# Optimization experiments

Hardware: AMD Instinct MI355X
Metric: run time of the kernel (lower is better)

The kernel has to match this reference:

```python
import jax, jax.numpy as jnp
import numpy as np

IN_FEAT, HIDDEN, OUT_FEAT = 2048, 1024, 2048
CODEBOOK_DIM, NUM_CODES = 32, 256
B, S = 4, 4096


def setup_inputs() -> dict:
    key = jax.random.key(0)
    ks = jax.random.split(key, 10)
    sc = lambda fan_in: 1.0 / np.sqrt(fan_in)
    return {
        "x": jax.random.normal(ks[0], (B, S, IN_FEAT), dtype=jnp.float32),
        # down: Linear(in_feat, hidden)
        "down_w": jax.random.normal(ks[1], (HIDDEN, IN_FEAT), dtype=jnp.float32) * sc(IN_FEAT),
        "down_b": jax.random.normal(ks[2], (HIDDEN,), dtype=jnp.float32) * sc(IN_FEAT),
        # VQ project_in: Linear(hidden, codebook_dim)
        "pin_w": jax.random.normal(ks[3], (CODEBOOK_DIM, HIDDEN), dtype=jnp.float32) * sc(HIDDEN),
        "pin_b": jax.random.normal(ks[4], (CODEBOOK_DIM,), dtype=jnp.float32) * sc(HIDDEN),
        # codebook embeddings
        "codebook": jax.random.normal(ks[5], (NUM_CODES, CODEBOOK_DIM), dtype=jnp.float32),
        # VQ project_out: Linear(codebook_dim, hidden)
        "pout_w": jax.random.normal(ks[6], (HIDDEN, CODEBOOK_DIM), dtype=jnp.float32) * sc(CODEBOOK_DIM),
        "pout_b": jax.random.normal(ks[7], (HIDDEN,), dtype=jnp.float32) * sc(CODEBOOK_DIM),
        # up: Linear(hidden, out_feat)
        "up_w": jax.random.normal(ks[8], (OUT_FEAT, HIDDEN), dtype=jnp.float32) * sc(HIDDEN),
        "up_b": jax.random.normal(ks[9], (OUT_FEAT,), dtype=jnp.float32) * sc(HIDDEN),
    }


def reference(x, down_w, down_b, pin_w, pin_b, codebook, pout_w, pout_b, up_w, up_b):
    # down-proj: [B,S,in] -> [B,S,hidden]
    h = jnp.einsum("bsi,hi->bsh", x, down_w) + down_b
    # VQ project_in: [B,S,hidden] -> [B,S,codebook_dim]
    z = jnp.einsum("bsh,ch->bsc", h, pin_w) + pin_b
    # squared euclidean distances to codebook: [B,S,num_codes]
    dist = (
        jnp.sum(z * z, axis=-1, keepdims=True)
        - 2.0 * jnp.einsum("bsc,nc->bsn", z, codebook)
        + jnp.sum(codebook * codebook, axis=-1)
    )
    indices = jnp.argmin(dist, axis=-1)  # [B,S] int
    quant = codebook[indices]            # [B,S,codebook_dim]
    # straight-through estimator
    quant = z + jax.lax.stop_gradient(quant - z)
    # VQ project_out: -> [B,S,hidden]
    hq = jnp.einsum("bsc,hc->bsh", quant, pout_w) + pout_b
    # up-proj: -> [B,S,out]
    out = jnp.einsum("bsh,oh->bso", hq, up_w) + up_b
    commit_loss = jnp.zeros((), dtype=x.dtype)  # commitment_weight = 0
    return jnp.clip(out, -1.0, 1.0), indices, commit_loss
```

## Files before the change

kernel.cpp:

```cpp
#include <hip/hip_runtime.h>

#define TOK   16384
#define INFT  2048
#define HID   1024
#define CBD   32
#define NC    256
#define OUTF  2048
#define KB    4

#define WS_UPWT   0
#define WS_ZPART  0
#define WS_PART1  2097152
#define WS_T      2097152
#define WS_WFT    3145728
#define WS_BF     3211264
#define WS_BPART  3211296
#define WS_PART2  3311648

__global__ __launch_bounds__(256) void k_stage1(
    const float* __restrict__ up_w, const float* __restrict__ pin_w,
    const float* __restrict__ pin_b, const float* __restrict__ down_w,
    const float* __restrict__ down_b, float* __restrict__ ws) {
    int bid = blockIdx.x, tid = threadIdx.x;
    if (bid < 2048) {
        __shared__ float tile[32][33];
        float* up_wT = ws + WS_UPWT;
        int h0 = (bid & 31) * 32;
        int o0 = (bid >> 5) * 32;
        int tx = tid & 31, ty = tid >> 5;
        #pragma unroll
        for (int j = 0; j < 32; j += 8)
            tile[ty + j][tx] = up_w[(o0 + ty + j) * HID + h0 + tx];
        __syncthreads();
        #pragma unroll
        for (int j = 0; j < 32; j += 8)
            up_wT[(h0 + ty + j) * OUTF + o0 + tx] = tile[tx][ty + j];
    } else if (bid < 2176) {
        float* part1 = ws + WS_PART1;
        int b  = bid - 2048;
        int i  = (b & 7) * 256 + tid;
        int k0 = (b >> 3) * 64;
        float acc[32];
        #pragma unroll
        for (int c = 0; c < 32; c++) acc[c] = 0.f;
        #pragma unroll 4
        for (int j = 0; j < 64; j++) {
            float xv = down_w[(k0 + j) * 2048 + i];
            #pragma unroll
            for (int c = 0; c < 32; c++)
                acc[c] = fmaf(pin_w[c * HID + k0 + j], xv, acc[c]);
        }
        #pragma unroll
        for (int c = 0; c < 32; c++)
            part1[((b >> 3) * 32 + c) * 2048 + i] = acc[c];
    } else {
        __shared__ float red[256];
        float* bf = ws + WS_BF;
        int c = tid >> 3, seg = tid & 7;
        float s = 0.f;
        #pragma unroll 8
        for (int k = seg * 128; k < seg * 128 + 128; k++)
            s = fmaf(pin_w[c * HID + k], down_b[k], s);
        red[tid] = s;
        __syncthreads();
        if (tid < 32) {
            float t = pin_b[tid];
            #pragma unroll
            for (int q = 0; q < 8; q++) t += red[tid * 8 + q];
            bf[tid] = t;
        }
    }
}

__global__ __launch_bounds__(256) void k_stage2(
    const float* __restrict__ pout_w, const float* __restrict__ pout_b,
    const float* __restrict__ up_b, float* __restrict__ ws) {
    int bid = blockIdx.x, tid = threadIdx.x;
    if (bid < 256) {
        const float* part1 = ws + WS_PART1;
        float* WfT = ws + WS_WFT;
        int f = bid * 256 + tid;
        int i = f & 2047, c = f >> 11;
        float s = 0.f;
        #pragma unroll
        for (int b = 0; b < 16; b++) s += part1[b * 65536 + c * 2048 + i];
        WfT[i * 32 + c] = s;
    } else {
        const float* up_wT = ws + WS_UPWT;
        float* part2 = ws + WS_PART2;
        float* bpart = ws + WS_BPART;
        int b  = bid - 256;
        int i  = (b & 7) * 256 + tid;
        int hc = b >> 3;
        int k0 = hc * 128;
        float acc[32];
        #pragma unroll
        for (int c = 0; c < 32; c++) acc[c] = 0.f;
        float accb = 0.f;
        #pragma unroll 4
        for (int j = 0; j < 128; j++) {
            float xv = up_wT[(k0 + j) * 2048 + i];
            accb = fmaf(pout_b[k0 + j], xv, accb);
            #pragma unroll
            for (int c = 0; c < 32; c++)
                acc[c] = fmaf(pout_w[(k0 + j) * 32 + c], xv, acc[c]);
        }
        #pragma unroll
        for (int c = 0; c < 32; c++)
            part2[(hc * 32 + c) * 2048 + i] = acc[c];
        bpart[hc * 2048 + i] = accb + (hc == 0 ? up_b[i] : 0.f);
    }
}

__global__ __launch_bounds__(256) void k_stage3(
    const float* __restrict__ x, const float* __restrict__ cb,
    float* __restrict__ ws) {
    __shared__ float4 xs[64 * 33 + 1];
    int bid = blockIdx.x, tid = threadIdx.x;
    if (bid < 64) {
        const float* part2 = ws + WS_PART2;
        const float* bpart = ws + WS_BPART;
        float* T = ws + WS_T;
        int o  = (bid & 7) * 256 + tid;
        int n0 = (bid >> 3) * 32;
        float u[32];
        #pragma unroll
        for (int c = 0; c < 32; c++) {
            float s = 0.f;
            #pragma unroll
            for (int kc = 0; kc < 8; kc++)
                s += part2[(kc * 32 + c) * 2048 + o];
            u[c] = s;
        }
        float bsum = 0.f;
        #pragma unroll
        for (int hc = 0; hc < 8; hc++) bsum += bpart[hc * 2048 + o];
        for (int n = n0; n < n0 + 32; n++) {
            float s = bsum;
            #pragma unroll
            for (int c = 0; c < 32; c++)
                s = fmaf(cb[n * 32 + c], u[c], s);
            T[n * 2048 + o] = s;
        }
    } else {
        const float* WfT = ws + WS_WFT;
        float* zpart = ws + WS_ZPART;
        int b    = bid - 64;
        int lane = tid & 63;
        int w    = __builtin_amdgcn_readfirstlane(tid >> 6);
        int m0   = (b & 255) * 64;
        int kb   = b >> 8;

        float acc[32];
        #pragma unroll
        for (int c = 0; c < 32; c++) acc[c] = 0.f;

        for (int sc = 0; sc < 4; sc++) {
            int k0 = kb * 512 + sc * 128;
            #pragma unroll
            for (int j = 0; j < 8; j++) {
                int f = j * 256 + tid;
                int t = f >> 5, q = f & 31;
                xs[t * 33 + q] = *(const float4*)(x + (size_t)(m0 + t) * 2048 + k0 + q * 4);
            }
            __syncthreads();
            const float* wr = WfT + (size_t)(k0 + w * 32) * 32;
            #pragma unroll 2
            for (int j = 0; j < 8; j++) {
                float4 xv = xs[lane * 33 + w * 8 + j];
                #pragma unroll
                for (int c = 0; c < 32; c++) {
                    acc[c] = fmaf(wr[(j * 4 + 0) * 32 + c], xv.x, acc[c]);
                    acc[c] = fmaf(wr[(j * 4 + 1) * 32 + c], xv.y, acc[c]);
                    acc[c] = fmaf(wr[(j * 4 + 2) * 32 + c], xv.z, acc[c]);
                    acc[c] = fmaf(wr[(j * 4 + 3) * 32 + c], xv.w, acc[c]);
                }
            }
            __syncthreads();
        }

        float* rp = (float*)xs;
        #pragma unroll
        for (int c = 0; c < 32; c++)
            rp[(w * 64 + lane) * 33 + c] = acc[c];
        __syncthreads();
        int t  = tid >> 2;
        int cq = (tid & 3) * 8;
        float s[8];
        #pragma unroll
        for (int j = 0; j < 8; j++) {
            float v = rp[(0 * 64 + t) * 33 + cq + j];
            #pragma unroll
            for (int ww = 1; ww < 4; ww++) v += rp[(ww * 64 + t) * 33 + cq + j];
            s[j] = v;
        }
        float* zp = zpart + ((size_t)kb * TOK + m0 + t) * 32 + cq;
        *(float4*)zp       = make_float4(s[0], s[1], s[2], s[3]);
        *(float4*)(zp + 4) = make_float4(s[4], s[5], s[6], s[7]);
    }
}

__global__ __launch_bounds__(256) void k_stage4(
    const float* __restrict__ cb, const float* __restrict__ ws,
    float* __restrict__ out, float* __restrict__ idx_f, float* __restrict__ loss) {
    __shared__ float z_s[64 * 36];
    __shared__ float cbs[256 * 36];
    __shared__ float cbn[256];
    __shared__ float red_d[256];
    __shared__ int   red_i[256];
    __shared__ int   idx_s[64];

    const float* zpart = ws + WS_ZPART;
    const float* bf    = ws + WS_BF;
    const float* T     = ws + WS_T;

    int tid  = threadIdx.x;
    int lane = tid & 63;
    int w    = __builtin_amdgcn_readfirstlane(tid >> 6);
    int m0   = blockIdx.x * 64;

    #pragma unroll
    for (int i = 0; i < 8; i++) {
        int f = i * 256 + tid;
        int t = f >> 5, c = f & 31;
        float s = bf[c];
        #pragma unroll
        for (int kb = 0; kb < KB; kb++)
            s += zpart[((size_t)kb * TOK + m0 + t) * 32 + c];
        z_s[t * 36 + c] = s;
    }
    #pragma unroll
    for (int j = 0; j < 8; j++) {
        int f = j * 256 + tid;
        int n = f >> 3, q = f & 7;
        float4 v = *(const float4*)(cb + n * 32 + q * 4);
        cbs[n * 36 + q * 4 + 0] = v.x;
        cbs[n * 36 + q * 4 + 1] = v.y;
        cbs[n * 36 + q * 4 + 2] = v.z;
        cbs[n * 36 + q * 4 + 3] = v.w;
    }
    __syncthreads();
    {
        float s = 0.f;
        #pragma unroll
        for (int q = 0; q < 8; q++) {
            float4 v = *(const float4*)(&cbs[tid * 36 + q * 4]);
            s += v.x * v.x + v.y * v.y + v.z * v.z + v.w * v.w;
        }
        cbn[tid] = s;
    }
    __syncthreads();

    float z[32];
    #pragma unroll
    for (int q = 0; q < 8; q++) {
        float4 v = *(const float4*)(&z_s[lane * 36 + q * 4]);
        z[q * 4 + 0] = v.x; z[q * 4 + 1] = v.y; z[q * 4 + 2] = v.z; z[q * 4 + 3] = v.w;
    }
    float bd = 3.4e38f; int bi = 0;
    for (int t = 0; t < 64; t++) {
        int n = w * 64 + t;
        float s = 0.f;
        #pragma unroll
        for (int q = 0; q < 8; q++) {
            float4 v = *(const float4*)(&cbs[n * 36 + q * 4]);
            s = fmaf(v.x, z[q * 4 + 0], s);
            s = fmaf(v.y, z[q * 4 + 1], s);
            s = fmaf(v.z, z[q * 4 + 2], s);
            s = fmaf(v.w, z[q * 4 + 3], s);
        }
        float d = fmaf(-2.f, s, cbn[n]);
        if (d < bd) { bd = d; bi = n; }
    }
    red_d[w * 64 + lane] = bd;
    red_i[w * 64 + lane] = bi;
    __syncthreads();
    if (tid < 64) {
        float d0 = red_d[tid]; int i0 = red_i[tid];
        #pragma unroll
        for (int ww = 1; ww < 4; ww++) {
            float d1 = red_d[ww * 64 + tid];
            int   i1 = red_i[ww * 64 + tid];
            if (d1 < d0) { d0 = d1; i0 = i1; }
        }
        idx_s[tid] = i0;
        idx_f[m0 + tid] = (float)i0;
    }
    __syncthreads();

    const float4* T4 = (const float4*)T;
    float4* O4 = (float4*)(out + (size_t)m0 * 2048);
    #pragma unroll 2
    for (int r = 0; r < 64; r++) {
        int n = idx_s[r];
        const float4* Tr = T4 + (size_t)n * 512;
        float4 v0 = Tr[tid];
        float4 v1 = Tr[256 + tid];
        v0.x = fminf(fmaxf(v0.x, -1.f), 1.f);
        v0.y = fminf(fmaxf(v0.y, -1.f), 1.f);
        v0.z = fminf(fmaxf(v0.z, -1.f), 1.f);
        v0.w = fminf(fmaxf(v0.w, -1.f), 1.f);
        v1.x = fminf(fmaxf(v1.x, -1.f), 1.f);
        v1.y = fminf(fmaxf(v1.y, -1.f), 1.f);
        v1.z = fminf(fmaxf(v1.z, -1.f), 1.f);
        v1.w = fminf(fmaxf(v1.w, -1.f), 1.f);
        O4[(size_t)r * 512 + tid]       = v0;
        O4[(size_t)r * 512 + 256 + tid] = v1;
    }
    if (blockIdx.x == 0 && tid == 0) *loss = 0.f;
}

extern "C" void kernel_launch(void* const* d_in, const int* in_sizes, int n_in,
                              void* d_out, int out_size, void* d_ws, size_t ws_size,
                              hipStream_t stream) {
    const float* x      = (const float*)d_in[0];
    const float* down_w = (const float*)d_in[1];
    const float* down_b = (const float*)d_in[2];
    const float* pin_w  = (const float*)d_in[3];
    const float* pin_b  = (const float*)d_in[4];
    const float* cb     = (const float*)d_in[5];
    const float* pout_w = (const float*)d_in[6];
    const float* pout_b = (const float*)d_in[7];
    const float* up_w   = (const float*)d_in[8];
    const float* up_b   = (const float*)d_in[9];

    float* ws = (float*)d_ws;
    float* out_f  = (float*)d_out;
    float* idx_f  = out_f + (size_t)TOK * OUTF;
    float* loss_f = idx_f + TOK;

    k_stage1<<<2177, 256, 0, stream>>>(up_w, pin_w, pin_b, down_w, down_b, ws);
    k_stage2<<<320,  256, 0, stream>>>(pout_w, pout_b, up_b, ws);
    k_stage3<<<1088, 256, 0, stream>>>(x, cb, ws);
    k_stage4<<<256,  256, 0, stream>>>(cb, ws, out_f, idx_f, loss_f);
}
```

Before: 391.3 us.

## Fuse z-projection GEMM with argmin/gather kernel and register-prefetch x tiles

Splits the former stage3 into a small table-building kernel and merges the fused x·Wf projection into the argmin/gather kernel, so each block computes its full 2048-long reduction itself instead of writing split-K partials to workspace. The x tile for the next chunk is prefetched into registers while the current chunk is computed. This removes the zpart round-trip and one split-K reduction, but cuts the projection grid from 1024 blocks to 256, which means less parallelism and latency hiding on a GPU with many compute units.

```diff
diff --git a/kernel.cpp b/kernel.cpp
--- a/kernel.cpp
+++ b/kernel.cpp
@@ -6,10 +6,8 @@
 #define CBD   32
 #define NC    256
 #define OUTF  2048
-#define KB    4
 
 #define WS_UPWT   0
-#define WS_ZPART  0
 #define WS_PART1  2097152
 #define WS_T      2097152
 #define WS_WFT    3145728
@@ -112,59 +110,103 @@
     }
 }
 
-__global__ __launch_bounds__(256) void k_stage3(
+__global__ __launch_bounds__(256) void k_table(
+    const float* __restrict__ cb, float* __restrict__ ws) {
+    const float* part2 = ws + WS_PART2;
+    const float* bpart = ws + WS_BPART;
+    float* T = ws + WS_T;
+    int bid = blockIdx.x, tid = threadIdx.x;
+    int o  = (bid & 7) * 256 + tid;
+    int n0 = (bid >> 3) * 32;
+    float u[32];
+    #pragma unroll
+    for (int c = 0; c < 32; c++) {
+        float s = 0.f;
+        #pragma unroll
+        for (int kc = 0; kc < 8; kc++)
+            s += part2[(kc * 32 + c) * 2048 + o];
+        u[c] = s;
+    }
+    float bsum = 0.f;
+    #pragma unroll
+    for (int hc = 0; hc < 8; hc++) bsum += bpart[hc * 2048 + o];
+    for (int n = n0; n < n0 + 32; n++) {
+        float s = bsum;
+        #pragma unroll
+        for (int c = 0; c < 32; c++)
+            s = fmaf(cb[n * 32 + c], u[c], s);
+        T[n * 2048 + o] = s;
+    }
+}
+
+__global__ __launch_bounds__(256) void k_main(
     const float* __restrict__ x, const float* __restrict__ cb,
-    float* __restrict__ ws) {
-    __shared__ float4 xs[64 * 33 + 1];
-    int bid = blockIdx.x, tid = threadIdx.x;
-    if (bid < 64) {
-        const float* part2 = ws + WS_PART2;
-        const float* bpart = ws + WS_BPART;
-        float* T = ws + WS_T;
-        int o  = (bid & 7) * 256 + tid;
-        int n0 = (bid >> 3) * 32;
-        float u[32];
-        #pragma unroll
-        for (int c = 0; c < 32; c++) {
-            float s = 0.f;
-            #pragma unroll
-            for (int kc = 0; kc < 8; kc++)
-                s += part2[(kc * 32 + c) * 2048 + o];
-            u[c] = s;
-        }
-        float bsum = 0.f;
-        #pragma unroll
-        for (int hc = 0; hc < 8; hc++) bsum += bpart[hc * 2048 + o];
-        for (int n = n0; n < n0 + 32; n++) {
-            float s = bsum;
-            #pragma unroll
-            for (int c = 0; c < 32; c++)
-                s = fmaf(cb[n * 32 + c], u[c], s);
-            T[n * 2048 + o] = s;
-        }
-    } else {
-        const float* WfT = ws + WS_WFT;
-        float* zpart = ws + WS_ZPART;
-        int b    = bid - 64;
-        int lane = tid & 63;
-        int w    = __builtin_amdgcn_readfirstlane(tid >> 6);
-        int m0   = (b & 255) * 64;
-        int kb   = b >> 8;
-
-        float acc[32];
-        #pragma unroll
-        for (int c = 0; c < 32; c++) acc[c] = 0.f;
-
+    const float* __restrict__ ws, float* __restrict__ out,
+    float* __restrict__ idx_f, float* __restrict__ loss) {
+    __shared__ __align__(16) char pool[49408];
+    float4* xs   = (float4*)pool;
+    float*  cbs  = (float*)pool;
+    float*  z_s  = (float*)(pool + 36864);
+    float*  cbn  = (float*)(pool + 46080);
+    float*  red_d = (float*)(pool + 47104);
+    int*    red_i = (int*)(pool + 48128);
+    int*    idx_s = (int*)(pool + 49152);
+
+    const float* WfT = ws + WS_WFT;
+    const float* bf  = ws + WS_BF;
+    const float* T   = ws + WS_T;
+
+    int tid  = threadIdx.x;
+    int lane = tid & 63;
+    int w    = __builtin_amdgcn_readfirstlane(tid >> 6);
+    int m0   = blockIdx.x * 64;
+    const float* xb = x + (size_t)m0 * 2048;
+
+    int tt = tid >> 2;
+    int cq = (tid & 3) * 8;
+
+    float bfv[8];
+    {
+        float4 b0 = *(const float4*)(bf + cq);
+        float4 b1 = *(const float4*)(bf + cq + 4);
+        bfv[0] = b0.x; bfv[1] = b0.y; bfv[2] = b0.z; bfv[3] = b0.w;
+        bfv[4] = b1.x; bfv[5] = b1.y; bfv[6] = b1.z; bfv[7] = b1.w;
+    }
+
+    float acc[32];
+    #pragma unroll
+    for (int c = 0; c < 32; c++) acc[c] = 0.f;
+    float stotal[8];
+
+    float4 r[8];
+    #pragma unroll
+    for (int j = 0; j < 8; j++) {
+        int f = j * 256 + tid;
+        int t = f >> 5, q = f & 31;
+        r[j] = *(const float4*)(xb + (size_t)t * 2048 + q * 4);
+    }
+
+    for (int kb = 0; kb < 4; kb++) {
         for (int sc = 0; sc < 4; sc++) {
-            int k0 = kb * 512 + sc * 128;
+            int ch = kb * 4 + sc;
+            __syncthreads();
             #pragma unroll
             for (int j = 0; j < 8; j++) {
                 int f = j * 256 + tid;
                 int t = f >> 5, q = f & 31;
-                xs[t * 33 + q] = *(const float4*)(x + (size_t)(m0 + t) * 2048 + k0 + q * 4);
+                xs[t * 33 + q] = r[j];
             }
             __syncthreads();
-            const float* wr = WfT + (size_t)(k0 + w * 32) * 32;
+            if (ch < 15) {
+                int k0n = (ch + 1) * 128;
+                #pragma unroll
+                for (int j = 0; j < 8; j++) {
+                    int f = j * 256 + tid;
+                    int t = f >> 5, q = f & 31;
+                    r[j] = *(const float4*)(xb + (size_t)t * 2048 + k0n + q * 4);
+                }
+            }
+            const float* wr = WfT + (size_t)(ch * 128 + w * 32) * 32;
             #pragma unroll 2
             for (int j = 0; j < 8; j++) {
                 float4 xv = xs[lane * 33 + w * 8 + j];
@@ -176,59 +218,29 @@
                     acc[c] = fmaf(wr[(j * 4 + 3) * 32 + c], xv.w, acc[c]);
                 }
             }
-            __syncthreads();
-        }
-
+        }
+        __syncthreads();
         float* rp = (float*)xs;
         #pragma unroll
         for (int c = 0; c < 32; c++)
             rp[(w * 64 + lane) * 33 + c] = acc[c];
         __syncthreads();
-        int t  = tid >> 2;
-        int cq = (tid & 3) * 8;
-        float s[8];
         #pragma unroll
         for (int j = 0; j < 8; j++) {
-            float v = rp[(0 * 64 + t) * 33 + cq + j];
-            #pragma unroll
-            for (int ww = 1; ww < 4; ww++) v += rp[(ww * 64 + t) * 33 + cq + j];
-            s[j] = v;
-        }
-        float* zp = zpart + ((size_t)kb * TOK + m0 + t) * 32 + cq;
-        *(float4*)zp       = make_float4(s[0], s[1], s[2], s[3]);
-        *(float4*)(zp + 4) = make_float4(s[4], s[5], s[6], s[7]);
-    }
-}
-
-__global__ __launch_bounds__(256) void k_stage4(
-    const float* __restrict__ cb, const float* __restrict__ ws,
-    float* __restrict__ out, float* __restrict__ idx_f, float* __restrict__ loss) {
-    __shared__ float z_s[64 * 36];
-    __shared__ float cbs[256 * 36];
-    __shared__ float cbn[256];
-    __shared__ float red_d[256];
-    __shared__ int   red_i[256];
-    __shared__ int   idx_s[64];
-
-    const float* zpart = ws + WS_ZPART;
-    const float* bf    = ws + WS_BF;
-    const float* T     = ws + WS_T;
-
-    int tid  = threadIdx.x;
-    int lane = tid & 63;
-    int w    = __builtin_amdgcn_readfirstlane(tid >> 6);
-    int m0   = blockIdx.x * 64;
-
-    #pragma unroll
-    for (int i = 0; i < 8; i++) {
-        int f = i * 256 + tid;
-        int t = f >> 5, c = f & 31;
-        float s = bf[c];
-        #pragma unroll
-        for (int kb = 0; kb < KB; kb++)
-            s += zpart[((size_t)kb * TOK + m0 + t) * 32 + c];
-        z_s[t * 36 + c] = s;
-    }
+            float v = rp[(0 * 64 + tt) * 33 + cq + j];
+            #pragma unroll
+            for (int ww = 1; ww < 4; ww++) v += rp[(ww * 64 + tt) * 33 + cq + j];
+            float base = (kb == 0) ? bfv[j] : stotal[j];
+            stotal[j] = base + v;
+        }
+        #pragma unroll
+        for (int c = 0; c < 32; c++) acc[c] = 0.f;
+    }
+
+    *(float4*)(z_s + tt * 36 + cq)     = make_float4(stotal[0], stotal[1], stotal[2], stotal[3]);
+    *(float4*)(z_s + tt * 36 + cq + 4) = make_float4(stotal[4], stotal[5], stotal[6], stotal[7]);
+    __syncthreads();
+
     #pragma unroll
     for (int j = 0; j < 8; j++) {
         int f = j * 256 + tid;
@@ -291,8 +303,8 @@
     const float4* T4 = (const float4*)T;
     float4* O4 = (float4*)(out + (size_t)m0 * 2048);
     #pragma unroll 2
-    for (int r = 0; r < 64; r++) {
-        int n = idx_s[r];
+    for (int rr = 0; rr < 64; rr++) {
+        int n = idx_s[rr];
         const float4* Tr = T4 + (size_t)n * 512;
         float4 v0 = Tr[tid];
         float4 v1 = Tr[256 + tid];
@@ -304,8 +316,8 @@
         v1.y = fminf(fmaxf(v1.y, -1.f), 1.f);
         v1.z = fminf(fmaxf(v1.z, -1.f), 1.f);
         v1.w = fminf(fmaxf(v1.w, -1.f), 1.f);
-        O4[(size_t)r * 512 + tid]       = v0;
-        O4[(size_t)r * 512 + 256 + tid] = v1;
+        O4[(size_t)rr * 512 + tid]       = v0;
+        O4[(size_t)rr * 512 + 256 + tid] = v1;
     }
     if (blockIdx.x == 0 && tid == 0) *loss = 0.f;
 }
@@ -331,6 +343,6 @@
 
     k_stage1<<<2177, 256, 0, stream>>>(up_w, pin_w, pin_b, down_w, down_b, ws);
     k_stage2<<<320,  256, 0, stream>>>(pout_w, pout_b, up_b, ws);
-    k_stage3<<<1088, 256, 0, stream>>>(x, cb, ws);
-    k_stage4<<<256,  256, 0, stream>>>(cb, ws, out_f, idx_f, loss_f);
-}
+    k_table<<<64,   256, 0, stream>>>(cb, ws);
+    k_main<<<256,   256, 0, stream>>>(x, cb, ws, out_f, idx_f, loss_f);
+}
```

New measurement: 543.9 us. +39.0%, slower.

## Split table and z-GEMM kernels, prefetch x tiles into registers

Applied to the files above, without the earlier changes.

The fused stage3 kernel, which branched on block id between building the output table and running the x·Wf GEMM, becomes two separate kernels. The GEMM kernel now loads the next 128-wide slice of x into registers while computing on the current slice in shared memory, a register double-buffering scheme. It also sets launch_bounds occupancy hint 4 and uses a 2D grid. This aims to hide global load latency and remove branch divergence between roles. The cost is higher register pressure and an extra kernel launch, and the small table kernel no longer overlaps with the GEMM.

```diff
diff --git a/kernel.cpp b/kernel.cpp
--- a/kernel.cpp
+++ b/kernel.cpp
@@ -112,96 +112,114 @@
     }
 }
 
-__global__ __launch_bounds__(256) void k_stage3(
-    const float* __restrict__ x, const float* __restrict__ cb,
-    float* __restrict__ ws) {
+__global__ __launch_bounds__(256) void k_table(
+    const float* __restrict__ cb, float* __restrict__ ws) {
+    const float* part2 = ws + WS_PART2;
+    const float* bpart = ws + WS_BPART;
+    float* T = ws + WS_T;
+    int bid = blockIdx.x, tid = threadIdx.x;
+    int o  = (bid & 7) * 256 + tid;
+    int n0 = (bid >> 3) * 32;
+    float u[32];
+    #pragma unroll
+    for (int c = 0; c < 32; c++) {
+        float s = 0.f;
+        #pragma unroll
+        for (int kc = 0; kc < 8; kc++)
+            s += part2[(kc * 32 + c) * 2048 + o];
+        u[c] = s;
+    }
+    float bsum = 0.f;
+    #pragma unroll
+    for (int hc = 0; hc < 8; hc++) bsum += bpart[hc * 2048 + o];
+    for (int n = n0; n < n0 + 32; n++) {
+        float s = bsum;
+        #pragma unroll
+        for (int c = 0; c < 32; c++)
+            s = fmaf(cb[n * 32 + c], u[c], s);
+        T[n * 2048 + o] = s;
+    }
+}
+
+__global__ __launch_bounds__(256, 4) void k_zgemm(
+    const float* __restrict__ x, const float* __restrict__ WfT,
+    float* __restrict__ zpart) {
     __shared__ float4 xs[64 * 33 + 1];
-    int bid = blockIdx.x, tid = threadIdx.x;
-    if (bid < 64) {
-        const float* part2 = ws + WS_PART2;
-        const float* bpart = ws + WS_BPART;
-        float* T = ws + WS_T;
-        int o  = (bid & 7) * 256 + tid;
-        int n0 = (bid >> 3) * 32;
-        float u[32];
-        #pragma unroll
-        for (int c = 0; c < 32; c++) {
-            float s = 0.f;
-            #pragma unroll
-            for (int kc = 0; kc < 8; kc++)
-                s += part2[(kc * 32 + c) * 2048 + o];
-            u[c] = s;
-        }
-        float bsum = 0.f;
-        #pragma unroll
-        for (int hc = 0; hc < 8; hc++) bsum += bpart[hc * 2048 + o];
-        for (int n = n0; n < n0 + 32; n++) {
-            float s = bsum;
-            #pragma unroll
-            for (int c = 0; c < 32; c++)
-                s = fmaf(cb[n * 32 + c], u[c], s);
-            T[n * 2048 + o] = s;
-        }
-    } else {
-        const float* WfT = ws + WS_WFT;
-        float* zpart = ws + WS_ZPART;
-        int b    = bid - 64;
-        int lane = tid & 63;
-        int w    = __builtin_amdgcn_readfirstlane(tid >> 6);
-        int m0   = (b & 255) * 64;
-        int kb   = b >> 8;
-
-        float acc[32];
-        #pragma unroll
-        for (int c = 0; c < 32; c++) acc[c] = 0.f;
-
-        for (int sc = 0; sc < 4; sc++) {
-            int k0 = kb * 512 + sc * 128;
+    int tid  = threadIdx.x;
+    int lane = tid & 63;
+    int w    = __builtin_amdgcn_readfirstlane(tid >> 6);
+    int m0   = blockIdx.x * 64;
+    int kb   = blockIdx.y;
+    const float* xb = x + (size_t)m0 * 2048 + kb * 512;
+
+    float acc[32];
+    #pragma unroll
+    for (int c = 0; c < 32; c++) acc[c] = 0.f;
+
+    float4 r[8];
+    #pragma unroll
+    for (int j = 0; j < 8; j++) {
+        int f = j * 256 + tid;
+        int t = f >> 5, q = f & 31;
+        r[j] = *(const float4*)(xb + (size_t)t * 2048 + q * 4);
+    }
+
+    for (int sc = 0; sc < 4; sc++) {
+        __syncthreads();
+        #pragma unroll
+        for (int j = 0; j < 8; j++) {
+            int f = j * 256 + tid;
+            int t = f >> 5, q = f & 31;
+            xs[t * 33 + q] = r[j];
+        }
+        __syncthreads();
+        if (sc < 3) {
+            int k0n = (sc + 1) * 128;
             #pragma unroll
             for (int j = 0; j < 8; j++) {
                 int f = j * 256 + tid;
                 int t = f >> 5, q = f & 31;
-                xs[t * 33 + q] = *(const float4*)(x + (size_t)(m0 + t) * 2048 + k0 + q * 4);
+                r[j] = *(const float4*)(xb + (size_t)t * 2048 + k0n + q * 4);
             }
-            __syncthreads();
-            const float* wr = WfT + (size_t)(k0 + w * 32) * 32;
-            #pragma unroll 2
-            for (int j = 0; j < 8; j++) {
-                float4 xv = xs[lane * 33 + w * 8 + j];
-                #pragma unroll
-                for (int c = 0; c < 32; c++) {
-                    acc[c] = fmaf(wr[(j * 4 + 0) * 32 + c], xv.x, acc[c]);
-                    acc[c] = fmaf(wr[(j * 4 + 1) * 32 + c], xv.y, acc[c]);
-                    acc[c] = fmaf(wr[(j * 4 + 2) * 32 + c], xv.z, acc[c]);
-                    acc[c] = fmaf(wr[(j * 4 + 3) * 32 + c], xv.w, acc[c]);
-                }
+        }
+        const float* wr = WfT + (size_t)(kb * 512 + sc * 128 + w * 32) * 32;
+        #pragma unroll 2
+        for (int j = 0; j < 8; j++) {
+            float4 xv = xs[lane * 33 + w * 8 + j];
+            #pragma unroll
+            for (int c = 0; c < 32; c++) {
+                acc[c] = fmaf(wr[(j * 4 + 0) * 32 + c], xv.x, acc[c]);
+                acc[c] = fmaf(wr[(j * 4 + 1) * 32 + c], xv.y, acc[c]);
+                acc[c] = fmaf(wr[(j * 4 + 2) * 32 + c], xv.z, acc[c]);
+                acc[c] = fmaf(wr[(j * 4 + 3) * 32 + c], xv.w, acc[c]);
             }
-            __syncthreads();
-        }
-
-        float* rp = (float*)xs;
-        #pragma unroll
-        for (int c = 0; c < 32; c++)
-            rp[(w * 64 + lane) * 33 + c] = acc[c];
-        __syncthreads();
-        int t  = tid >> 2;
-        int cq = (tid & 3) * 8;
-        float s[8];
-        #pragma unroll
-        for (int j = 0; j < 8; j++) {
-            float v = rp[(0 * 64 + t) * 33 + cq + j];
-            #pragma unroll
-            for (int ww = 1; ww < 4; ww++) v += rp[(ww * 64 + t) * 33 + cq + j];
-            s[j] = v;
-        }
-        float* zp = zpart + ((size_t)kb * TOK + m0 + t) * 32 + cq;
-        *(float4*)zp       = make_float4(s[0], s[1], s[2], s[3]);
-        *(float4*)(zp + 4) = make_float4(s[4], s[5], s[6], s[7]);
-    }
+        }
+    }
+
+    __syncthreads();
+    float* rp = (float*)xs;
+    #pragma unroll
+    for (int c = 0; c < 32; c++)
+        rp[(w * 64 + lane) * 33 + c] = acc[c];
+    __syncthreads();
+    int t  = tid >> 2;
+    int cq = (tid & 3) * 8;
+    float s[8];
+    #pragma unroll
+    for (int j = 0; j < 8; j++) {
+        float v = rp[(0 * 64 + t) * 33 + cq + j];
+        #pragma unroll
+        for (int ww = 1; ww < 4; ww++) v += rp[(ww * 64 + t) * 33 + cq + j];
+        s[j] = v;
+    }
+    float* zp = zpart + ((size_t)kb * TOK + m0 + t) * 32 + cq;
+    *(float4*)zp       = make_float4(s[0], s[1], s[2], s[3]);
+    *(float4*)(zp + 4) = make_float4(s[4], s[5], s[6], s[7]);
 }
 
 __global__ __launch_bounds__(256) void k_stage4(
-    const float* __restrict__ cb, const float* __restrict__ ws,
+    const float* __restrict__ zpart, const float* __restrict__ bf,
+    const float* __restrict__ T, const float* __restrict__ cb,
     float* __restrict__ out, float* __restrict__ idx_f, float* __restrict__ loss) {
     __shared__ float z_s[64 * 36];
     __shared__ float cbs[256 * 36];
@@ -209,10 +227,6 @@
     __shared__ float red_d[256];
     __shared__ int   red_i[256];
     __shared__ int   idx_s[64];
-
-    const float* zpart = ws + WS_ZPART;
-    const float* bf    = ws + WS_BF;
-    const float* T     = ws + WS_T;
 
     int tid  = threadIdx.x;
     int lane = tid & 63;
@@ -291,8 +305,8 @@
     const float4* T4 = (const float4*)T;
     float4* O4 = (float4*)(out + (size_t)m0 * 2048);
     #pragma unroll 2
-    for (int r = 0; r < 64; r++) {
-        int n = idx_s[r];
+    for (int rr = 0; rr < 64; rr++) {
+        int n = idx_s[rr];
         const float4* Tr = T4 + (size_t)n * 512;
         float4 v0 = Tr[tid];
         float4 v1 = Tr[256 + tid];
@@ -304,8 +318,8 @@
         v1.y = fminf(fmaxf(v1.y, -1.f), 1.f);
         v1.z = fminf(fmaxf(v1.z, -1.f), 1.f);
         v1.w = fminf(fmaxf(v1.w, -1.f), 1.f);
-        O4[(size_t)r * 512 + tid]       = v0;
-        O4[(size_t)r * 512 + 256 + tid] = v1;
+        O4[(size_t)rr * 512 + tid]       = v0;
+        O4[(size_t)rr * 512 + 256 + tid] = v1;
     }
     if (blockIdx.x == 0 && tid == 0) *loss = 0.f;
 }
@@ -325,12 +339,18 @@
     const float* up_b   = (const float*)d_in[9];
 
     float* ws = (float*)d_ws;
+    float* zpart = ws + WS_ZPART;
+    float* WfT   = ws + WS_WFT;
+    float* bf    = ws + WS_BF;
+    float* T     = ws + WS_T;
+
     float* out_f  = (float*)d_out;
     float* idx_f  = out_f + (size_t)TOK * OUTF;
     float* loss_f = idx_f + TOK;
 
     k_stage1<<<2177, 256, 0, stream>>>(up_w, pin_w, pin_b, down_w, down_b, ws);
     k_stage2<<<320,  256, 0, stream>>>(pout_w, pout_b, up_b, ws);
-    k_stage3<<<1088, 256, 0, stream>>>(x, cb, ws);
-    k_stage4<<<256,  256, 0, stream>>>(cb, ws, out_f, idx_f, loss_f);
-}
+    k_table<<<64,    256, 0, stream>>>(cb, ws);
+    k_zgemm<<<dim3(256, KB), 256, 0, stream>>>(x, WfT, zpart);
+    k_stage4<<<256,  256, 0, stream>>>(zpart, bf, T, cb, out_f, idx_f, loss_f);
+}
```

New measurement: 451.2 us. 15.3% more time.

## Double-buffer x tiles via direct global-to-LDS loads with XOR swizzle

Applied to the files above, without the earlier changes.

The x-projection GEMV in the third stage now stages x chunks straight into LDS with global_load_lds and double-buffers them, so the load of the next 128-column chunk overlaps compute on the current one. A padded layout is replaced by an XOR swizzle to avoid bank conflicts, and launch bounds request 4 blocks per CU. The costs are twice the shared memory for the x tiles and some register pressure from the occupancy hint. Stage 4 now takes explicit pointers instead of workspace offsets.

```diff
diff --git a/kernel.cpp b/kernel.cpp
--- a/kernel.cpp
+++ b/kernel.cpp
@@ -112,10 +112,25 @@
     }
 }
 
-__global__ __launch_bounds__(256) void k_stage3(
+#define STAGE_CHUNK(dstbuf, ch_)                                              \
+    {                                                                         \
+        const float* sb_ = xb + (ch_) * 128;                                  \
+        _Pragma("unroll")                                                     \
+        for (int j = 0; j < 8; j++) {                                         \
+            int row_  = (w * 8 + j) * 2 + (lane >> 5);                        \
+            int clog_ = (lane & 31) ^ (row_ & 31);                            \
+            const float* srcp_ = sb_ + (size_t)row_ * 2048 + clog_ * 4;       \
+            __builtin_amdgcn_global_load_lds(                                 \
+                (const __attribute__((address_space(1))) void*)srcp_,         \
+                (__attribute__((address_space(3))) void*)((dstbuf) + (w * 8 + j) * 64), \
+                16, 0, 0);                                                    \
+        }                                                                     \
+    }
+
+__global__ __launch_bounds__(256, 4) void k_zmain(
     const float* __restrict__ x, const float* __restrict__ cb,
-    float* __restrict__ ws) {
-    __shared__ float4 xs[64 * 33 + 1];
+    const float* __restrict__ WfT, float* __restrict__ ws) {
+    __shared__ float4 buf2[2][64 * 32];
     int bid = blockIdx.x, tid = threadIdx.x;
     if (bid < 64) {
         const float* part2 = ws + WS_PART2;
@@ -142,66 +157,66 @@
                 s = fmaf(cb[n * 32 + c], u[c], s);
             T[n * 2048 + o] = s;
         }
-    } else {
-        const float* WfT = ws + WS_WFT;
-        float* zpart = ws + WS_ZPART;
-        int b    = bid - 64;
-        int lane = tid & 63;
-        int w    = __builtin_amdgcn_readfirstlane(tid >> 6);
-        int m0   = (b & 255) * 64;
-        int kb   = b >> 8;
-
-        float acc[32];
-        #pragma unroll
-        for (int c = 0; c < 32; c++) acc[c] = 0.f;
-
-        for (int sc = 0; sc < 4; sc++) {
-            int k0 = kb * 512 + sc * 128;
-            #pragma unroll
-            for (int j = 0; j < 8; j++) {
-                int f = j * 256 + tid;
-                int t = f >> 5, q = f & 31;
-                xs[t * 33 + q] = *(const float4*)(x + (size_t)(m0 + t) * 2048 + k0 + q * 4);
+        return;
+    }
+
+    float* zpart = ws + WS_ZPART;
+    int b    = bid - 64;
+    int lane = tid & 63;
+    int w    = __builtin_amdgcn_readfirstlane(tid >> 6);
+    int m0   = (b & 255) * 64;
+    int kb   = b >> 8;
+    const float* xb = x + (size_t)m0 * 2048 + kb * 512;
+    int l5 = lane & 31;
+
+    float acc[32];
+    #pragma unroll
+    for (int c = 0; c < 32; c++) acc[c] = 0.f;
+
+    STAGE_CHUNK(buf2[0], 0);
+    __syncthreads();
+
+    for (int ch = 0; ch < 4; ch++) {
+        if (ch < 3) STAGE_CHUNK(buf2[(ch + 1) & 1], ch + 1);
+        const float4* bcur = buf2[ch & 1];
+        const float* wr = WfT + (size_t)(kb * 512 + ch * 128 + w * 32) * 32;
+        #pragma unroll 2
+        for (int j = 0; j < 8; j++) {
+            float4 xv = bcur[lane * 32 + ((w * 8 + j) ^ l5)];
+            #pragma unroll
+            for (int c = 0; c < 32; c++) {
+                acc[c] = fmaf(wr[(j * 4 + 0) * 32 + c], xv.x, acc[c]);
+                acc[c] = fmaf(wr[(j * 4 + 1) * 32 + c], xv.y, acc[c]);
+                acc[c] = fmaf(wr[(j * 4 + 2) * 32 + c], xv.z, acc[c]);
+                acc[c] = fmaf(wr[(j * 4 + 3) * 32 + c], xv.w, acc[c]);
             }
-            __syncthreads();
-            const float* wr = WfT + (size_t)(k0 + w * 32) * 32;
-            #pragma unroll 2
-            for (int j = 0; j < 8; j++) {
-                float4 xv = xs[lane * 33 + w * 8 + j];
-                #pragma unroll
-                for (int c = 0; c < 32; c++) {
-                    acc[c] = fmaf(wr[(j * 4 + 0) * 32 + c], xv.x, acc[c]);
-                    acc[c] = fmaf(wr[(j * 4 + 1) * 32 + c], xv.y, acc[c]);
-                    acc[c] = fmaf(wr[(j * 4 + 2) * 32 + c], xv.z, acc[c]);
-                    acc[c] = fmaf(wr[(j * 4 + 3) * 32 + c], xv.w, acc[c]);
-                }
-            }
-            __syncthreads();
-        }
-
-        float* rp = (float*)xs;
-        #pragma unroll
-        for (int c = 0; c < 32; c++)
-            rp[(w * 64 + lane) * 33 + c] = acc[c];
+        }
         __syncthreads();
-        int t  = tid >> 2;
-        int cq = (tid & 3) * 8;
-        float s[8];
-        #pragma unroll
-        for (int j = 0; j < 8; j++) {
-            float v = rp[(0 * 64 + t) * 33 + cq + j];
-            #pragma unroll
-            for (int ww = 1; ww < 4; ww++) v += rp[(ww * 64 + t) * 33 + cq + j];
-            s[j] = v;
-        }
-        float* zp = zpart + ((size_t)kb * TOK + m0 + t) * 32 + cq;
-        *(float4*)zp       = make_float4(s[0], s[1], s[2], s[3]);
-        *(float4*)(zp + 4) = make_float4(s[4], s[5], s[6], s[7]);
-    }
+    }
+
+    float* rp = (float*)buf2;
+    #pragma unroll
+    for (int c = 0; c < 32; c++)
+        rp[(w * 64 + lane) * 33 + c] = acc[c];
+    __syncthreads();
+    int t  = tid >> 2;
+    int cq = (tid & 3) * 8;
+    float s[8];
+    #pragma unroll
+    for (int j = 0; j < 8; j++) {
+        float v = rp[(0 * 64 + t) * 33 + cq + j];
+        #pragma unroll
+        for (int ww = 1; ww < 4; ww++) v += rp[(ww * 64 + t) * 33 + cq + j];
+        s[j] = v;
+    }
+    float* zp = zpart + ((size_t)kb * TOK + m0 + t) * 32 + cq;
+    *(float4*)zp       = make_float4(s[0], s[1], s[2], s[3]);
+    *(float4*)(zp + 4) = make_float4(s[4], s[5], s[6], s[7]);
 }
 
 __global__ __launch_bounds__(256) void k_stage4(
-    const float* __restrict__ cb, const float* __restrict__ ws,
+    const float* __restrict__ zpart, const float* __restrict__ bf,
+    const float* __restrict__ T, const float* __restrict__ cb,
     float* __restrict__ out, float* __restrict__ idx_f, float* __restrict__ loss) {
     __shared__ float z_s[64 * 36];
     __shared__ float cbs[256 * 36];
@@ -209,10 +224,6 @@
     __shared__ float red_d[256];
     __shared__ int   red_i[256];
     __shared__ int   idx_s[64];
-
-    const float* zpart = ws + WS_ZPART;
-    const float* bf    = ws + WS_BF;
-    const float* T     = ws + WS_T;
 
     int tid  = threadIdx.x;
     int lane = tid & 63;
@@ -291,8 +302,8 @@
     const float4* T4 = (const float4*)T;
     float4* O4 = (float4*)(out + (size_t)m0 * 2048);
     #pragma unroll 2
-    for (int r = 0; r < 64; r++) {
-        int n = idx_s[r];
+    for (int rr = 0; rr < 64; rr++) {
+        int n = idx_s[rr];
         const float4* Tr = T4 + (size_t)n * 512;
         float4 v0 = Tr[tid];
         float4 v1 = Tr[256 + tid];
@@ -304,8 +315,8 @@
         v1.y = fminf(fmaxf(v1.y, -1.f), 1.f);
         v1.z = fminf(fmaxf(v1.z, -1.f), 1.f);
         v1.w = fminf(fmaxf(v1.w, -1.f), 1.f);
-        O4[(size_t)r * 512 + tid]       = v0;
-        O4[(size_t)r * 512 + 256 + tid] = v1;
+        O4[(size_t)rr * 512 + tid]       = v0;
+        O4[(size_t)rr * 512 + 256 + tid] = v1;
     }
     if (blockIdx.x == 0 && tid == 0) *loss = 0.f;
 }
@@ -325,12 +336,17 @@
     const float* up_b   = (const float*)d_in[9];
 
     float* ws = (float*)d_ws;
+    float* zpart = ws + WS_ZPART;
+    float* WfT   = ws + WS_WFT;
+    float* bf    = ws + WS_BF;
+    float* T     = ws + WS_T;
+
     float* out_f  = (float*)d_out;
     float* idx_f  = out_f + (size_t)TOK * OUTF;
     float* loss_f = idx_f + TOK;
 
     k_stage1<<<2177, 256, 0, stream>>>(up_w, pin_w, pin_b, down_w, down_b, ws);
     k_stage2<<<320,  256, 0, stream>>>(pout_w, pout_b, up_b, ws);
-    k_stage3<<<1088, 256, 0, stream>>>(x, cb, ws);
-    k_stage4<<<256,  256, 0, stream>>>(cb, ws, out_f, idx_f, loss_f);
-}
+    k_zmain<<<1088,  256, 0, stream>>>(x, cb, WfT, ws);
+    k_stage4<<<256,  256, 0, stream>>>(zpart, bf, T, cb, out_f, idx_f, loss_f);
+}
```

Result: no change. 387.9 us (-0.9%).
